# Kernel optimization log

Measured on AMD Instinct MI355X. Metric: run time of the kernel, lower is better.

Reference implementation:

```python
import jax, jax.numpy as jnp
import numpy as np

SIGMA = 1.0

def setup_inputs() -> dict:
    key = jax.random.key(0)
    kx, ky = jax.random.split(key)
    x = jax.random.normal(kx, (8192, 256), dtype=jnp.float32)
    y = jax.random.normal(ky, (8192, 256), dtype=jnp.float32)
    return {"x": x, "y": y}

def reference(x, y):
    x2 = jnp.sum(x * x, axis=-1)            # [N]
    y2 = jnp.sum(y * y, axis=-1)            # [M]
    d2 = x2[:, None] + y2[None, :] - 2.0 * (x @ y.T)  # [N, M]
    d2 = jnp.maximum(d2, 0.0)
    k = jnp.exp(-d2 / (2.0 * SIGMA ** 2))
    # original: exp(...)[None].sum(dim=0).mean() == mean over all N*M entries
    return jnp.mean(k)
```

## Files before the change

### kernel.cpp

```cpp
#include <hip/hip_runtime.h>

#define NROWS 8192
#define DIM   256

typedef __bf16 bf16x8 __attribute__((ext_vector_type(8)));
typedef __bf16 bf16x4 __attribute__((ext_vector_type(4)));
typedef float  f32x4  __attribute__((ext_vector_type(4)));

typedef __attribute__((address_space(3))) char lds_char;
typedef __attribute__((address_space(1))) const char glob_char;

#define LOG2E  1.4426950408889634f
#define NEG_HALF_LOG2E (-0.7213475204444817f)

__global__ __launch_bounds__(256) void prep_kernel(
    const float* __restrict__ x, const float* __restrict__ y,
    __bf16* __restrict__ xb, __bf16* __restrict__ yb,
    float* __restrict__ px, float* __restrict__ py,
    float* __restrict__ out)
{
    int tid  = threadIdx.x;
    int lane = tid & 63;
    int w    = tid >> 6;
    int row  = blockIdx.x * 4 + w;
    bool isx = row < NROWS;
    int r    = isx ? row : row - NROWS;
    const float* src = (isx ? x : y) + (size_t)r * DIM;
    float4 v = reinterpret_cast<const float4*>(src)[lane];
    float sq = v.x*v.x + v.y*v.y + v.z*v.z + v.w*v.w;
    #pragma unroll
    for (int off = 32; off; off >>= 1) sq += __shfl_xor(sq, off);
    bf16x4 h;
    h[0] = (__bf16)v.x; h[1] = (__bf16)v.y; h[2] = (__bf16)v.z; h[3] = (__bf16)v.w;
    __bf16* dst = (isx ? xb : yb) + (size_t)r * DIM + lane * 4;
    *reinterpret_cast<bf16x4*>(dst) = h;
    if (lane == 0) (isx ? px : py)[r] = NEG_HALF_LOG2E * sq;
    if (blockIdx.x == 0 && tid == 0) out[0] = 0.0f;
}

__global__ __launch_bounds__(512, 1) void rbf_gemm_kernel(
    const __bf16* __restrict__ xb, const __bf16* __restrict__ yb,
    const float* __restrict__ px, const float* __restrict__ py,
    float* __restrict__ out)
{
    __shared__ char smem[131072];
    __shared__ float red[8];

    int tid  = threadIdx.x;
    int lane = tid & 63;
    int wv   = tid >> 6;
    int wm   = wv >> 2;
    int wn   = wv & 3;
    int bm   = blockIdx.x & 31;
    int bn   = blockIdx.x >> 5;
    int h    = lane >> 4;
    int l15  = lane & 15;

    f32x4 acc[8][4];
    #pragma unroll
    for (int m = 0; m < 8; ++m)
        #pragma unroll
        for (int n = 0; n < 4; ++n)
            acc[m][n] = (f32x4){0.f, 0.f, 0.f, 0.f};

    auto stage = [&](int buf, int kt) {
        size_t ktoff = (size_t)kt * 128;
        #pragma unroll
        for (int i = 0; i < 4; ++i) {
            int lin = i * 8192 + tid * 16;
            int row = lin >> 7;
            int kbs = (lin & 127) ^ ((row & 7) << 4);
            size_t gA = (size_t)(bm * 256 + row) * 512 + ktoff + kbs;
            size_t gB = (size_t)(bn * 256 + row) * 512 + ktoff + kbs;
            int ldsoff = buf * 65536 + i * 8192 + wv * 1024;
            __builtin_amdgcn_global_load_lds(
                (glob_char*)((const char*)xb + gA),
                (lds_char*)(smem + ldsoff), 16, 0, 0);
            __builtin_amdgcn_global_load_lds(
                (glob_char*)((const char*)yb + gB),
                (lds_char*)(smem + 32768 + ldsoff), 16, 0, 0);
        }
    };

    auto compute = [&](int buf) {
        const char* Ab = smem + buf * 65536;
        const char* Bb = Ab + 32768;
        #pragma unroll
        for (int kk = 0; kk < 2; ++kk) {
            bf16x8 af[8], bfr[4];
            #pragma unroll
            for (int n = 0; n < 4; ++n) {
                int row = wn * 64 + n * 16 + l15;
                int kb  = (kk * 64 + h * 16) ^ ((row & 7) << 4);
                bfr[n] = *reinterpret_cast<const bf16x8*>(Bb + row * 128 + kb);
            }
            #pragma unroll
            for (int m = 0; m < 8; ++m) {
                int row = wm * 128 + m * 16 + l15;
                int kb  = (kk * 64 + h * 16) ^ ((row & 7) << 4);
                af[m] = *reinterpret_cast<const bf16x8*>(Ab + row * 128 + kb);
            }
            #pragma unroll
            for (int m = 0; m < 8; ++m)
                #pragma unroll
                for (int n = 0; n < 4; ++n)
                    acc[m][n] = __builtin_amdgcn_mfma_f32_16x16x32_bf16(
                        af[m], bfr[n], acc[m][n], 0, 0, 0);
        }
    };

    stage(0, 0);
    __syncthreads();
    #pragma unroll
    for (int kt = 0; kt < 4; ++kt) {
        int cur = kt & 1;
        if (kt < 3) stage(cur ^ 1, kt + 1);
        compute(cur);
        __syncthreads();
    }

    float lsum = 0.f;
    int colbase = bn * 256 + wn * 64 + l15;
    int rowbase = bm * 256 + wm * 128 + h * 4;
    float py4[4];
    #pragma unroll
    for (int n = 0; n < 4; ++n) py4[n] = py[colbase + n * 16];
    #pragma unroll
    for (int m = 0; m < 8; ++m) {
        #pragma unroll
        for (int r = 0; r < 4; ++r) {
            float pxv = px[rowbase + m * 16 + r];
            #pragma unroll
            for (int n = 0; n < 4; ++n)
                lsum += exp2f(fmaf(acc[m][n][r], LOG2E, pxv + py4[n]));
        }
    }
    #pragma unroll
    for (int off = 32; off; off >>= 1) lsum += __shfl_xor(lsum, off);
    if (lane == 0) red[wv] = lsum;
    __syncthreads();
    if (tid == 0) {
        float s = (red[0] + red[1] + red[2] + red[3] +
                   red[4] + red[5] + red[6] + red[7]) * 1.4901161193847656e-08f;
        atomicAdd(out, s);
    }
}

extern "C" void kernel_launch(void* const* d_in, const int* in_sizes, int n_in,
                              void* d_out, int out_size, void* d_ws, size_t ws_size,
                              hipStream_t stream) {
    const float* x = (const float*)d_in[0];
    const float* y = (const float*)d_in[1];
    float* out = (float*)d_out;
    char* ws = (char*)d_ws;
    __bf16* xb = (__bf16*)ws;
    __bf16* yb = (__bf16*)(ws + (size_t)4 * 1024 * 1024);
    float*  px = (float*)(ws + (size_t)8 * 1024 * 1024);
    float*  py = (float*)(ws + (size_t)8 * 1024 * 1024 + 32 * 1024);

    hipLaunchKernelGGL(prep_kernel, dim3(4096), dim3(256), 0, stream,
                       x, y, xb, yb, px, py, out);
    hipLaunchKernelGGL(rbf_gemm_kernel, dim3(1024), dim3(512), 0, stream,
                       xb, yb, px, py, out);
}
```

Baseline: 115.7 us.

## Interleave quadrant MFMAs with fine-grained async staging in GEMM mainloop

Restructures the bf16 GEMM mainloop into four MFMA quadrants per k-tile. LDS fragment loads and global-to-LDS staging of the tile two steps ahead are interleaved between quadrants, with raw s_barrier and explicit vmcnt waits replacing __syncthreads. Staging is split into per-matrix half units so each LDS region is refilled as soon as the quadrants that read it finish. s_setprio is raised around MFMA bursts. This aims to hide global load latency and cut barrier stalls, at the risk of correctness bugs from the hand-managed waitcnt and buffer reuse.

```diff
diff --git a/kernel.cpp b/kernel.cpp
--- a/kernel.cpp
+++ b/kernel.cpp
@@ -12,6 +12,8 @@
 
 #define LOG2E  1.4426950408889634f
 #define NEG_HALF_LOG2E (-0.7213475204444817f)
+
+#define BAR() asm volatile("s_barrier" ::: "memory")
 
 __global__ __launch_bounds__(256) void prep_kernel(
     const float* __restrict__ x, const float* __restrict__ y,
@@ -63,60 +65,88 @@
         for (int n = 0; n < 4; ++n)
             acc[m][n] = (f32x4){0.f, 0.f, 0.f, 0.f};
 
-    auto stage = [&](int buf, int kt) {
-        size_t ktoff = (size_t)kt * 128;
+    auto stage_unit = [&](int buf, int kt, int matrix, int unit) {
+        const __bf16* src = matrix ? yb : xb;
+        int baserow = (matrix ? bn : bm) * 256;
         #pragma unroll
-        for (int i = 0; i < 4; ++i) {
-            int lin = i * 8192 + tid * 16;
-            int row = lin >> 7;
-            int kbs = (lin & 127) ^ ((row & 7) << 4);
-            size_t gA = (size_t)(bm * 256 + row) * 512 + ktoff + kbs;
-            size_t gB = (size_t)(bn * 256 + row) * 512 + ktoff + kbs;
-            int ldsoff = buf * 65536 + i * 8192 + wv * 1024;
+        for (int j = 0; j < 2; ++j) {
+            int lin = j * 8192 + tid * 16;
+            int off;
+            if (matrix == 0) off = unit * 8192 + lin + (lin >> 13) * 8192;
+            else             off = unit * 4096 + lin + (lin >> 12) * 4096;
+            int row = off >> 7;
+            int kb  = off & 127;
+            int kbs = kb ^ ((row & 7) << 4);
+            size_t g = (size_t)(baserow + row) * 512 + (size_t)kt * 128 + kbs;
             __builtin_amdgcn_global_load_lds(
-                (glob_char*)((const char*)xb + gA),
-                (lds_char*)(smem + ldsoff), 16, 0, 0);
-            __builtin_amdgcn_global_load_lds(
-                (glob_char*)((const char*)yb + gB),
-                (lds_char*)(smem + 32768 + ldsoff), 16, 0, 0);
+                (glob_char*)((const char*)src + g),
+                (lds_char*)(smem + buf * 65536 + matrix * 32768 + off), 16, 0, 0);
         }
     };
 
-    auto compute = [&](int buf) {
+    auto ldA = [&](int buf, int mbase, bf16x8* aF) {
         const char* Ab = smem + buf * 65536;
-        const char* Bb = Ab + 32768;
         #pragma unroll
-        for (int kk = 0; kk < 2; ++kk) {
-            bf16x8 af[8], bfr[4];
+        for (int m = 0; m < 4; ++m)
             #pragma unroll
-            for (int n = 0; n < 4; ++n) {
-                int row = wn * 64 + n * 16 + l15;
+            for (int kk = 0; kk < 2; ++kk) {
+                int row = wm * 128 + (mbase + m) * 16 + l15;
                 int kb  = (kk * 64 + h * 16) ^ ((row & 7) << 4);
-                bfr[n] = *reinterpret_cast<const bf16x8*>(Bb + row * 128 + kb);
+                aF[m * 2 + kk] = *reinterpret_cast<const bf16x8*>(Ab + row * 128 + kb);
             }
+    };
+    auto ldB = [&](int buf, int nbase, bf16x8* bF) {
+        const char* Bb = smem + buf * 65536 + 32768;
+        #pragma unroll
+        for (int n = 0; n < 2; ++n)
             #pragma unroll
-            for (int m = 0; m < 8; ++m) {
-                int row = wm * 128 + m * 16 + l15;
+            for (int kk = 0; kk < 2; ++kk) {
+                int row = wn * 64 + (nbase + n) * 16 + l15;
                 int kb  = (kk * 64 + h * 16) ^ ((row & 7) << 4);
-                af[m] = *reinterpret_cast<const bf16x8*>(Ab + row * 128 + kb);
+                bF[n * 2 + kk] = *reinterpret_cast<const bf16x8*>(Bb + row * 128 + kb);
             }
+    };
+    auto mmaq = [&](int mbase, int nbase, bf16x8* aF, bf16x8* bF) {
+        __builtin_amdgcn_s_setprio(1);
+        #pragma unroll
+        for (int m = 0; m < 4; ++m)
             #pragma unroll
-            for (int m = 0; m < 8; ++m)
+            for (int n = 0; n < 2; ++n)
                 #pragma unroll
-                for (int n = 0; n < 4; ++n)
-                    acc[m][n] = __builtin_amdgcn_mfma_f32_16x16x32_bf16(
-                        af[m], bfr[n], acc[m][n], 0, 0, 0);
-        }
+                for (int kk = 0; kk < 2; ++kk)
+                    acc[mbase + m][nbase + n] = __builtin_amdgcn_mfma_f32_16x16x32_bf16(
+                        aF[m * 2 + kk], bF[n * 2 + kk], acc[mbase + m][nbase + n], 0, 0, 0);
+        __builtin_amdgcn_s_setprio(0);
     };
 
-    stage(0, 0);
-    __syncthreads();
+    stage_unit(0, 0, 0, 0); stage_unit(0, 0, 1, 0);
+    stage_unit(0, 0, 1, 1); stage_unit(0, 0, 0, 1);
+    stage_unit(1, 1, 0, 0); stage_unit(1, 1, 1, 0);
+    stage_unit(1, 1, 1, 1); stage_unit(1, 1, 0, 1);
+    asm volatile("s_waitcnt vmcnt(8)" ::: "memory");
+    BAR();
+
     #pragma unroll
     for (int kt = 0; kt < 4; ++kt) {
-        int cur = kt & 1;
-        if (kt < 3) stage(cur ^ 1, kt + 1);
-        compute(cur);
-        __syncthreads();
+        int buf = kt & 1;
+        bf16x8 aF[8], bF0[4], bF1[4];
+        ldA(buf, 0, aF);
+        ldB(buf, 0, bF0);
+        mmaq(0, 0, aF, bF0);
+        BAR();
+        ldB(buf, 2, bF1);
+        if (kt < 2) { stage_unit(buf, kt + 2, 0, 0); stage_unit(buf, kt + 2, 1, 0); }
+        mmaq(0, 2, aF, bF1);
+        BAR();
+        ldA(buf, 4, aF);
+        if (kt < 2) stage_unit(buf, kt + 2, 1, 1);
+        mmaq(4, 2, aF, bF1);
+        BAR();
+        if (kt < 2) stage_unit(buf, kt + 2, 0, 1);
+        mmaq(4, 0, aF, bF0);
+        if (kt < 2)       asm volatile("s_waitcnt vmcnt(8)" ::: "memory");
+        else if (kt == 2) asm volatile("s_waitcnt vmcnt(0)" ::: "memory");
+        BAR();
     }
 
     float lsum = 0.f;
```

Result: no change. 113.5 us (-1.9%).

## Persist B tile in LDS and stream A through five-stage pipeline per block

Applied to the files above, without the earlier changes.

The GEMM kernel is restructured so each of 256 blocks keeps a 128-column slab of y resident in LDS and loops over eight 256-row tiles of x. Those x tiles are streamed through a 5-slot LDS ring using global_load_lds with explicit vmcnt waits and raw s_barrier, and fragments are double-buffered in registers. The exp epilogue runs per tile, reading px/py from LDS, and s_setprio is raised around the MFMA bursts. This targets global load redundancy and the exposed load latency of the old short 4-step K loop. In exchange the swizzle is dropped, which risks LDS bank conflicts, and the hand-counted waitcnts are fragile.

```diff
diff --git a/kernel.cpp b/kernel.cpp
--- a/kernel.cpp
+++ b/kernel.cpp
@@ -12,6 +12,8 @@
 
 #define LOG2E  1.4426950408889634f
 #define NEG_HALF_LOG2E (-0.7213475204444817f)
+
+#define BAR() asm volatile("s_barrier" ::: "memory")
 
 __global__ __launch_bounds__(256) void prep_kernel(
     const float* __restrict__ x, const float* __restrict__ y,
@@ -30,10 +32,10 @@
     float sq = v.x*v.x + v.y*v.y + v.z*v.z + v.w*v.w;
     #pragma unroll
     for (int off = 32; off; off >>= 1) sq += __shfl_xor(sq, off);
-    bf16x4 h;
-    h[0] = (__bf16)v.x; h[1] = (__bf16)v.y; h[2] = (__bf16)v.z; h[3] = (__bf16)v.w;
+    bf16x4 hh;
+    hh[0] = (__bf16)v.x; hh[1] = (__bf16)v.y; hh[2] = (__bf16)v.z; hh[3] = (__bf16)v.w;
     __bf16* dst = (isx ? xb : yb) + (size_t)r * DIM + lane * 4;
-    *reinterpret_cast<bf16x4*>(dst) = h;
+    *reinterpret_cast<bf16x4*>(dst) = hh;
     if (lane == 0) (isx ? px : py)[r] = NEG_HALF_LOG2E * sq;
     if (blockIdx.x == 0 && tid == 0) out[0] = 0.0f;
 }
@@ -43,98 +45,157 @@
     const float* __restrict__ px, const float* __restrict__ py,
     float* __restrict__ out)
 {
-    __shared__ char smem[131072];
-    __shared__ float red[8];
+    __shared__ __align__(16) char smem[156192];
+    float* pxl = (float*)(smem + 147456);
+    float* pyl = (float*)(smem + 155648);
+    float* red = (float*)(smem + 156160);
 
     int tid  = threadIdx.x;
     int lane = tid & 63;
     int wv   = tid >> 6;
-    int wm   = wv >> 2;
-    int wn   = wv & 3;
-    int bm   = blockIdx.x & 31;
-    int bn   = blockIdx.x >> 5;
+    int wm   = wv >> 1;
+    int wn   = wv & 1;
+    int c    = blockIdx.x & 7;
+    int bmg  = c >> 1;
+    int bn   = (blockIdx.x >> 3) * 2 + (c & 1);
     int h    = lane >> 4;
     int l15  = lane & 15;
-
-    f32x4 acc[8][4];
-    #pragma unroll
-    for (int m = 0; m < 8; ++m)
+    int abase = bmg * 2048;
+    int bbase = bn * 128;
+
+    f32x4 acc[4][4];
+    #pragma unroll
+    for (int m = 0; m < 4; ++m)
         #pragma unroll
         for (int n = 0; n < 4; ++n)
             acc[m][n] = (f32x4){0.f, 0.f, 0.f, 0.f};
 
-    auto stage = [&](int buf, int kt) {
-        size_t ktoff = (size_t)kt * 128;
-        #pragma unroll
-        for (int i = 0; i < 4; ++i) {
-            int lin = i * 8192 + tid * 16;
-            int row = lin >> 7;
-            int kbs = (lin & 127) ^ ((row & 7) << 4);
-            size_t gA = (size_t)(bm * 256 + row) * 512 + ktoff + kbs;
-            size_t gB = (size_t)(bn * 256 + row) * 512 + ktoff + kbs;
-            int ldsoff = buf * 65536 + i * 8192 + wv * 1024;
+    auto stageA = [&](int s, int g) {
+        int rowbase = abase + ((g >> 3) << 8);
+        int ktcol   = (g & 7) << 6;
+        char* dst0  = smem + 65536 + s * 16384;
+        #pragma unroll
+        for (int j = 0; j < 2; ++j) {
+            int e  = j * 512 + tid;
+            int hh = e >> 8, row = e & 255;
             __builtin_amdgcn_global_load_lds(
-                (glob_char*)((const char*)xb + gA),
-                (lds_char*)(smem + ldsoff), 16, 0, 0);
-            __builtin_amdgcn_global_load_lds(
-                (glob_char*)((const char*)yb + gB),
-                (lds_char*)(smem + 32768 + ldsoff), 16, 0, 0);
+                (glob_char*)((const char*)xb + (size_t)(rowbase + row) * 512 + ktcol + hh * 16),
+                (lds_char*)(dst0 + e * 16), 16, 0, 0);
         }
     };
 
-    auto compute = [&](int buf) {
-        const char* Ab = smem + buf * 65536;
-        const char* Bb = Ab + 32768;
-        #pragma unroll
-        for (int kk = 0; kk < 2; ++kk) {
-            bf16x8 af[8], bfr[4];
+    auto readA = [&](int s, bf16x8* a) {
+        const char* base = smem + 65536 + s * 16384 + h * 4096 + (wm * 64 + l15) * 16;
+        #pragma unroll
+        for (int mf = 0; mf < 4; ++mf)
+            a[mf] = *reinterpret_cast<const bf16x8*>(base + mf * 256);
+    };
+    auto readB = [&](int kt, bf16x8* b) {
+        const char* base = smem + kt * 8192 + h * 2048 + (wn * 64 + l15) * 16;
+        #pragma unroll
+        for (int nf = 0; nf < 4; ++nf)
+            b[nf] = *reinterpret_cast<const bf16x8*>(base + nf * 256);
+    };
+    auto mma = [&](bf16x8* a, bf16x8* b) {
+        __builtin_amdgcn_s_setprio(1);
+        #pragma unroll
+        for (int mf = 0; mf < 4; ++mf)
             #pragma unroll
-            for (int n = 0; n < 4; ++n) {
-                int row = wn * 64 + n * 16 + l15;
-                int kb  = (kk * 64 + h * 16) ^ ((row & 7) << 4);
-                bfr[n] = *reinterpret_cast<const bf16x8*>(Bb + row * 128 + kb);
+            for (int nf = 0; nf < 4; ++nf)
+                acc[mf][nf] = __builtin_amdgcn_mfma_f32_16x16x32_bf16(
+                    a[mf], b[nf], acc[mf][nf], 0, 0, 0);
+        __builtin_amdgcn_s_setprio(0);
+    };
+
+    float lsum = 0.f;
+    float py4[4];
+
+    auto epi = [&](int t) {
+        const float* pxt = pxl + t * 256 + wm * 64;
+        #pragma unroll
+        for (int mf = 0; mf < 4; ++mf) {
+            f32x4 pxv = *reinterpret_cast<const f32x4*>(pxt + mf * 16 + h * 4);
+            #pragma unroll
+            for (int r = 0; r < 4; ++r) {
+                float pv = pxv[r];
+                #pragma unroll
+                for (int nf = 0; nf < 4; ++nf)
+                    lsum += exp2f(fmaf(acc[mf][nf][r], LOG2E, pv + py4[nf]));
             }
             #pragma unroll
-            for (int m = 0; m < 8; ++m) {
-                int row = wm * 128 + m * 16 + l15;
-                int kb  = (kk * 64 + h * 16) ^ ((row & 7) << 4);
-                af[m] = *reinterpret_cast<const bf16x8*>(Ab + row * 128 + kb);
-            }
-            #pragma unroll
-            for (int m = 0; m < 8; ++m)
-                #pragma unroll
-                for (int n = 0; n < 4; ++n)
-                    acc[m][n] = __builtin_amdgcn_mfma_f32_16x16x32_bf16(
-                        af[m], bfr[n], acc[m][n], 0, 0, 0);
+            for (int nf = 0; nf < 4; ++nf)
+                acc[mf][nf] = (f32x4){0.f, 0.f, 0.f, 0.f};
         }
     };
 
-    stage(0, 0);
-    __syncthreads();
-    #pragma unroll
-    for (int kt = 0; kt < 4; ++kt) {
-        int cur = kt & 1;
-        if (kt < 3) stage(cur ^ 1, kt + 1);
-        compute(cur);
-        __syncthreads();
-    }
-
-    float lsum = 0.f;
-    int colbase = bn * 256 + wn * 64 + l15;
-    int rowbase = bm * 256 + wm * 128 + h * 4;
-    float py4[4];
-    #pragma unroll
-    for (int n = 0; n < 4; ++n) py4[n] = py[colbase + n * 16];
-    #pragma unroll
-    for (int m = 0; m < 8; ++m) {
-        #pragma unroll
-        for (int r = 0; r < 4; ++r) {
-            float pxv = px[rowbase + m * 16 + r];
-            #pragma unroll
-            for (int n = 0; n < 4; ++n)
-                lsum += exp2f(fmaf(acc[m][n][r], LOG2E, pxv + py4[n]));
-        }
-    }
+    if (wv == 0) {
+        #pragma unroll
+        for (int j = 0; j < 2; ++j)
+            __builtin_amdgcn_global_load_lds(
+                (glob_char*)((const char*)(py + bbase + j * 64) + lane * 4),
+                (lds_char*)((char*)pyl + j * 256 + lane * 4), 4, 0, 0);
+    }
+    #pragma unroll
+    for (int j = 0; j < 8; ++j) {
+        int e  = j * 512 + tid;
+        int kt = e >> 9, hh = (e >> 7) & 3, row = e & 127;
+        __builtin_amdgcn_global_load_lds(
+            (glob_char*)((const char*)yb + (size_t)(bbase + row) * 512 + kt * 64 + hh * 16),
+            (lds_char*)(smem + e * 16), 16, 0, 0);
+    }
+    __builtin_amdgcn_global_load_lds(
+        (glob_char*)((const char*)(px + abase) + tid * 16),
+        (lds_char*)((char*)pxl + tid * 16), 16, 0, 0);
+    stageA(0, 0); stageA(1, 1); stageA(2, 2); stageA(3, 3);
+    asm volatile("s_waitcnt vmcnt(4)" ::: "memory");
+    BAR();
+
+    #pragma unroll
+    for (int nf = 0; nf < 4; ++nf)
+        py4[nf] = pyl[wn * 64 + nf * 16 + l15];
+
+    bf16x8 aCur[4], bCur[4], aNxt[4], bNxt[4];
+    readA(0, aCur); readB(0, bCur);
+
+    int s1 = 1, s4 = 4;
+    int gg = 0;
+    #pragma unroll 1
+    for (int i = 0; i < 30; ++i) {
+        stageA(s4, gg + 4);
+        if (++s4 == 5) s4 = 0;
+        readA(s1, aNxt); readB((gg + 1) & 7, bNxt);
+        if (++s1 == 5) s1 = 0;
+        mma(aCur, bCur);
+        asm volatile("s_waitcnt vmcnt(4)" ::: "memory");
+        BAR();
+        ++gg;
+        stageA(s4, gg + 4);
+        if (++s4 == 5) s4 = 0;
+        readA(s1, aCur); readB((gg + 1) & 7, bCur);
+        if (++s1 == 5) s1 = 0;
+        mma(aNxt, bNxt);
+        if ((gg & 7) == 7) epi(gg >> 3);
+        asm volatile("s_waitcnt vmcnt(4)" ::: "memory");
+        BAR();
+        ++gg;
+    }
+
+    readA(s1, aNxt); readB(5, bNxt);
+    if (++s1 == 5) s1 = 0;
+    mma(aCur, bCur);
+    asm volatile("s_waitcnt vmcnt(2)" ::: "memory");
+    BAR();
+    readA(s1, aCur); readB(6, bCur);
+    if (++s1 == 5) s1 = 0;
+    mma(aNxt, bNxt);
+    asm volatile("s_waitcnt vmcnt(0)" ::: "memory");
+    BAR();
+    readA(s1, aNxt); readB(7, bNxt);
+    mma(aCur, bCur);
+    BAR();
+    mma(aNxt, bNxt);
+    epi(7);
+
     #pragma unroll
     for (int off = 32; off; off >>= 1) lsum += __shfl_xor(lsum, off);
     if (lane == 0) red[wv] = lsum;
@@ -160,6 +221,6 @@
 
     hipLaunchKernelGGL(prep_kernel, dim3(4096), dim3(256), 0, stream,
                        x, y, xb, yb, px, py, out);
-    hipLaunchKernelGGL(rbf_gemm_kernel, dim3(1024), dim3(512), 0, stream,
+    hipLaunchKernelGGL(rbf_gemm_kernel, dim3(256), dim3(512), 0, stream,
                        xb, yb, px, py, out);
 }
```

Result: slower. 127.9 us (+10.5%).

## Switch GEMM to FP8 MFMA with pre-permuted layout and smaller multi-occupancy tiles

Applied to the files above, without the earlier changes.

Inputs are quantized to FP8 e4m3 in the prep kernel, written in a k-permuted order so each lane's 16 bytes feed two 16x16x32 fp8 MFMAs, and the GEMM uses fp8 MFMA instead of bf16. Tiles shrink to 256x128 with 48KB LDS, launch bounds allow 4 blocks per CU, the grid doubles and block-to-tile mapping is swizzled for L2 reuse. This halves operand bytes and raises MFMA throughput and occupancy. The cost is much lower input precision, which could push the exp-kernel mean past tolerance.

```diff
diff --git a/kernel.cpp b/kernel.cpp
--- a/kernel.cpp
+++ b/kernel.cpp
@@ -1,11 +1,11 @@
 #include <hip/hip_runtime.h>
+#include <hip/hip_fp8.h>
 
 #define NROWS 8192
 #define DIM   256
 
-typedef __bf16 bf16x8 __attribute__((ext_vector_type(8)));
-typedef __bf16 bf16x4 __attribute__((ext_vector_type(4)));
-typedef float  f32x4  __attribute__((ext_vector_type(4)));
+typedef float f32x4 __attribute__((ext_vector_type(4)));
+typedef long  i64x2 __attribute__((ext_vector_type(2)));
 
 typedef __attribute__((address_space(3))) char lds_char;
 typedef __attribute__((address_space(1))) const char glob_char;
@@ -13,9 +13,24 @@
 #define LOG2E  1.4426950408889634f
 #define NEG_HALF_LOG2E (-0.7213475204444817f)
 
+__device__ __forceinline__ int pack4_fp8(float a, float b, float c, float d) {
+#if __has_builtin(__builtin_amdgcn_cvt_pk_fp8_f32)
+    int pk = __builtin_amdgcn_cvt_pk_fp8_f32(a, b, 0, false);
+    pk     = __builtin_amdgcn_cvt_pk_fp8_f32(c, d, pk, true);
+    return pk;
+#else
+    union { unsigned char by[4]; int i; } u;
+    u.by[0] = __hip_fp8_e4m3(a).__x;
+    u.by[1] = __hip_fp8_e4m3(b).__x;
+    u.by[2] = __hip_fp8_e4m3(c).__x;
+    u.by[3] = __hip_fp8_e4m3(d).__x;
+    return u.i;
+#endif
+}
+
 __global__ __launch_bounds__(256) void prep_kernel(
     const float* __restrict__ x, const float* __restrict__ y,
-    __bf16* __restrict__ xb, __bf16* __restrict__ yb,
+    unsigned char* __restrict__ xb, unsigned char* __restrict__ yb,
     float* __restrict__ px, float* __restrict__ py,
     float* __restrict__ out)
 {
@@ -30,109 +45,113 @@
     float sq = v.x*v.x + v.y*v.y + v.z*v.z + v.w*v.w;
     #pragma unroll
     for (int off = 32; off; off >>= 1) sq += __shfl_xor(sq, off);
-    bf16x4 h;
-    h[0] = (__bf16)v.x; h[1] = (__bf16)v.y; h[2] = (__bf16)v.z; h[3] = (__bf16)v.w;
-    __bf16* dst = (isx ? xb : yb) + (size_t)r * DIM + lane * 4;
-    *reinterpret_cast<bf16x4*>(dst) = h;
+
+    int pk = pack4_fp8(v.x, v.y, v.z, v.w);
+    int k0 = lane * 4;
+    int kt = k0 >> 6, q = k0 & 63;
+    int s  = q >> 5, hh = (q >> 3) & 3, j0 = q & 7;
+    int p0 = (kt << 6) + (hh << 4) + (s << 3) + j0;
+    unsigned char* dst = (isx ? xb : yb) + (size_t)r * DIM + p0;
+    *reinterpret_cast<int*>(dst) = pk;
+
     if (lane == 0) (isx ? px : py)[r] = NEG_HALF_LOG2E * sq;
     if (blockIdx.x == 0 && tid == 0) out[0] = 0.0f;
 }
 
-__global__ __launch_bounds__(512, 1) void rbf_gemm_kernel(
-    const __bf16* __restrict__ xb, const __bf16* __restrict__ yb,
+__global__ __launch_bounds__(512, 4) void rbf_gemm_kernel(
+    const unsigned char* __restrict__ xb, const unsigned char* __restrict__ yb,
     const float* __restrict__ px, const float* __restrict__ py,
     float* __restrict__ out)
 {
-    __shared__ char smem[131072];
+    __shared__ __align__(16) char smem[49152];
     __shared__ float red[8];
 
     int tid  = threadIdx.x;
     int lane = tid & 63;
     int wv   = tid >> 6;
-    int wm   = wv >> 2;
-    int wn   = wv & 3;
-    int bm   = blockIdx.x & 31;
-    int bn   = blockIdx.x >> 5;
+    int wm   = wv >> 1;
+    int wn   = wv & 1;
+    int b    = blockIdx.x;
+    int bm   = (b & 7) * 4 + (b >> 9);
+    int bn   = (b >> 3) & 63;
     int h    = lane >> 4;
     int l15  = lane & 15;
 
-    f32x4 acc[8][4];
+    f32x4 acc[4][4];
     #pragma unroll
-    for (int m = 0; m < 8; ++m)
+    for (int m = 0; m < 4; ++m)
         #pragma unroll
         for (int n = 0; n < 4; ++n)
             acc[m][n] = (f32x4){0.f, 0.f, 0.f, 0.f};
 
     auto stage = [&](int buf, int kt) {
-        size_t ktoff = (size_t)kt * 128;
+        char* base = smem + buf * 24576;
         #pragma unroll
-        for (int i = 0; i < 4; ++i) {
-            int lin = i * 8192 + tid * 16;
-            int row = lin >> 7;
-            int kbs = (lin & 127) ^ ((row & 7) << 4);
-            size_t gA = (size_t)(bm * 256 + row) * 512 + ktoff + kbs;
-            size_t gB = (size_t)(bn * 256 + row) * 512 + ktoff + kbs;
-            int ldsoff = buf * 65536 + i * 8192 + wv * 1024;
+        for (int j = 0; j < 2; ++j) {
+            int e = j * 512 + tid;
+            int hh = e >> 8, row = e & 255;
             __builtin_amdgcn_global_load_lds(
-                (glob_char*)((const char*)xb + gA),
-                (lds_char*)(smem + ldsoff), 16, 0, 0);
+                (glob_char*)((const char*)xb + (size_t)(bm * 256 + row) * 256 + kt * 64 + hh * 16),
+                (lds_char*)(base + e * 16), 16, 0, 0);
+        }
+        {
+            int e = tid;
+            int hh = e >> 7, row = e & 127;
             __builtin_amdgcn_global_load_lds(
-                (glob_char*)((const char*)yb + gB),
-                (lds_char*)(smem + 32768 + ldsoff), 16, 0, 0);
+                (glob_char*)((const char*)yb + (size_t)(bn * 128 + row) * 256 + kt * 64 + hh * 16),
+                (lds_char*)(base + 16384 + e * 16), 16, 0, 0);
         }
     };
 
     auto compute = [&](int buf) {
-        const char* Ab = smem + buf * 65536;
-        const char* Bb = Ab + 32768;
+        const char* Ab = smem + buf * 24576;
+        const char* Bb = Ab + 16384;
+        i64x2 aF[4], bF[4];
         #pragma unroll
-        for (int kk = 0; kk < 2; ++kk) {
-            bf16x8 af[8], bfr[4];
+        for (int mf = 0; mf < 4; ++mf)
+            aF[mf] = *reinterpret_cast<const i64x2*>(
+                Ab + h * 4096 + (wm * 64 + mf * 16 + l15) * 16);
+        #pragma unroll
+        for (int nf = 0; nf < 4; ++nf)
+            bF[nf] = *reinterpret_cast<const i64x2*>(
+                Bb + h * 2048 + (wn * 64 + nf * 16 + l15) * 16);
+        __builtin_amdgcn_s_setprio(1);
+        #pragma unroll
+        for (int mf = 0; mf < 4; ++mf)
             #pragma unroll
-            for (int n = 0; n < 4; ++n) {
-                int row = wn * 64 + n * 16 + l15;
-                int kb  = (kk * 64 + h * 16) ^ ((row & 7) << 4);
-                bfr[n] = *reinterpret_cast<const bf16x8*>(Bb + row * 128 + kb);
+            for (int nf = 0; nf < 4; ++nf) {
+                acc[mf][nf] = __builtin_amdgcn_mfma_f32_16x16x32_fp8_fp8(
+                    aF[mf][0], bF[nf][0], acc[mf][nf], 0, 0, 0);
+                acc[mf][nf] = __builtin_amdgcn_mfma_f32_16x16x32_fp8_fp8(
+                    aF[mf][1], bF[nf][1], acc[mf][nf], 0, 0, 0);
             }
-            #pragma unroll
-            for (int m = 0; m < 8; ++m) {
-                int row = wm * 128 + m * 16 + l15;
-                int kb  = (kk * 64 + h * 16) ^ ((row & 7) << 4);
-                af[m] = *reinterpret_cast<const bf16x8*>(Ab + row * 128 + kb);
-            }
-            #pragma unroll
-            for (int m = 0; m < 8; ++m)
-                #pragma unroll
-                for (int n = 0; n < 4; ++n)
-                    acc[m][n] = __builtin_amdgcn_mfma_f32_16x16x32_bf16(
-                        af[m], bfr[n], acc[m][n], 0, 0, 0);
-        }
+        __builtin_amdgcn_s_setprio(0);
     };
 
     stage(0, 0);
     __syncthreads();
     #pragma unroll
     for (int kt = 0; kt < 4; ++kt) {
-        int cur = kt & 1;
-        if (kt < 3) stage(cur ^ 1, kt + 1);
-        compute(cur);
+        int buf = kt & 1;
+        if (kt < 3) stage(buf ^ 1, kt + 1);
+        compute(buf);
         __syncthreads();
     }
 
     float lsum = 0.f;
-    int colbase = bn * 256 + wn * 64 + l15;
-    int rowbase = bm * 256 + wm * 128 + h * 4;
+    int colbase = bn * 128 + wn * 64 + l15;
+    int rowbase = bm * 256 + wm * 64 + h * 4;
     float py4[4];
     #pragma unroll
-    for (int n = 0; n < 4; ++n) py4[n] = py[colbase + n * 16];
+    for (int nf = 0; nf < 4; ++nf) py4[nf] = py[colbase + nf * 16];
     #pragma unroll
-    for (int m = 0; m < 8; ++m) {
+    for (int mf = 0; mf < 4; ++mf) {
         #pragma unroll
         for (int r = 0; r < 4; ++r) {
-            float pxv = px[rowbase + m * 16 + r];
+            float pv = px[rowbase + mf * 16 + r];
             #pragma unroll
-            for (int n = 0; n < 4; ++n)
-                lsum += exp2f(fmaf(acc[m][n][r], LOG2E, pxv + py4[n]));
+            for (int nf = 0; nf < 4; ++nf)
+                lsum += exp2f(fmaf(acc[mf][nf][r], LOG2E, pv + py4[nf]));
         }
     }
     #pragma unroll
@@ -153,13 +172,13 @@
     const float* y = (const float*)d_in[1];
     float* out = (float*)d_out;
     char* ws = (char*)d_ws;
-    __bf16* xb = (__bf16*)ws;
-    __bf16* yb = (__bf16*)(ws + (size_t)4 * 1024 * 1024);
-    float*  px = (float*)(ws + (size_t)8 * 1024 * 1024);
-    float*  py = (float*)(ws + (size_t)8 * 1024 * 1024 + 32 * 1024);
+    unsigned char* xb = (unsigned char*)ws;
+    unsigned char* yb = (unsigned char*)(ws + (size_t)2 * 1024 * 1024);
+    float* px = (float*)(ws + (size_t)4 * 1024 * 1024);
+    float* py = (float*)(ws + (size_t)4 * 1024 * 1024 + 32 * 1024);
 
     hipLaunchKernelGGL(prep_kernel, dim3(4096), dim3(256), 0, stream,
                        x, y, xb, yb, px, py, out);
-    hipLaunchKernelGGL(rbf_gemm_kernel, dim3(1024), dim3(512), 0, stream,
+    hipLaunchKernelGGL(rbf_gemm_kernel, dim3(2048), dim3(512), 0, stream,
                        xb, yb, px, py, out);
 }
```

Measured after the change: 116.1 us. Within noise of the previous version (+0.3%).
